# Kernel tuning notes

Hardware: AMD Instinct MI355X
Metric: run time of the kernel (lower is better)

The kernel has to match this reference:

```python
import jax, jax.numpy as jnp
import numpy as np
from jax import lax

IMG_W = 800.0
CONF_THRESHOLD = 0.5
MAX_MATCHES = 8
N_PROPOSALS = 65536
N_TARGETS = 128


def setup_inputs() -> dict:
    key = jax.random.key(0)
    ks = jax.random.split(key, 14)
    N, T = N_PROPOSALS, N_TARGETS
    # raw (pre-normalization) geometric scores: theta in [0, 360) deg,
    # start-point / distance errors in [0, 2*img_w) px (exercises the clamp branch)
    theta = jax.random.uniform(ks[0], (N, T), jnp.float32) * 360.0
    xys = jax.random.uniform(ks[1], (N, T), jnp.float32) * (2.0 * IMG_W)
    dist = jax.random.uniform(ks[2], (N, T), jnp.float32) * (2.0 * IMG_W)
    pos = jax.random.uniform(ks[3], (N, T), jnp.float32)
    neg = jax.random.uniform(ks[4], (N, T), jnp.float32)
    iou = jax.random.uniform(ks[5], (N, T), jnp.float32)
    targets = jax.random.uniform(ks[6], (T, 4), jnp.float32)
    # MatchNet: small MLP 6 -> 64 -> 32 -> 1 with ReLU hidden, sigmoid output
    W1 = jax.random.normal(ks[7], (6, 64), jnp.float32) * 0.3
    b1 = jnp.zeros((64,), jnp.float32)
    W2 = jax.random.normal(ks[8], (64, 32), jnp.float32) * 0.3
    b2 = jnp.zeros((32,), jnp.float32)
    W3 = jax.random.normal(ks[9], (32, 1), jnp.float32) * 0.3
    b3 = jnp.zeros((1,), jnp.float32)
    return {
        "theta_score_deep": theta, "start_xys_score_deep": xys,
        "distances_score_deep": dist, "pos_score_deep": pos,
        "neg_score_deep": neg, "iou_deep": iou, "targets": targets,
        "W1": W1, "b1": b1, "W2": W2, "b2": b2, "W3": W3, "b3": b3,
    }


def _norm(x, cap):
    # torch: x[x > cap] = cap; x = 1 - x / cap
    return 1.0 - jnp.minimum(x, cap) / cap


def _matchnet(feats, W1, b1, W2, b2, W3, b3):
    # feats: [N, T, 6] -> scores [N, T]
    h = jax.nn.relu(feats @ W1 + b1)
    h = jax.nn.relu(h @ W2 + b2)
    return jax.nn.sigmoid(h @ W3 + b3)[..., 0]


def reference(theta_score_deep, start_xys_score_deep, distances_score_deep,
              pos_score_deep, neg_score_deep, iou_deep, targets,
              W1, b1, W2, b2, W3, b3):
    theta = _norm(theta_score_deep, 180.0)
    xys = _norm(start_xys_score_deep, IMG_W)
    dist = _norm(distances_score_deep, IMG_W)
    feats = jnp.stack([theta, xys, dist, pos_score_deep, neg_score_deep, iou_deep],
                      axis=-1)                      # [N, T, 6]
    scores = _matchnet(feats, W1, b1, W2, b2, W3, b3)  # [N, T]
    scores = jnp.where(scores < CONF_THRESHOLD, 0.0, scores)
    # top-k proposals per target, fully batched over the target dim
    vals, idx = lax.top_k(scores.T, MAX_MATCHES)    # [T, K] each
    # the torch loop visits targets in descending order of targets[:, 1]
    order = jnp.argsort(-targets[:, 1], stable=True)  # [T]
    rows = idx[order].reshape(-1).astype(jnp.int32)   # [T*K]
    cols = jnp.repeat(order.astype(jnp.int32), MAX_MATCHES)  # [T*K]
    valid = (vals[order] > 0.0).reshape(-1)           # [T*K] bool
    # fixed-shape padded equivalent of the original's variable-length cat:
    # (rows[valid], cols[valid]) reproduces the torch output exactly
    return rows, cols, valid
```

## Files before the change

kernel.cpp:

```cpp
#include <hip/hip_runtime.h>


typedef unsigned int   u32;
typedef unsigned short u16;
typedef short s8v  __attribute__((ext_vector_type(8)));
typedef float f4v  __attribute__((ext_vector_type(4)));

#define N_PROP   65536
#define N_TGT    128
#define N_PAIR   (N_PROP * N_TGT)
#define CAP      4096
#define MARGIN   0.15f
#define NCHUNK   512

static __device__ __forceinline__ u32 packbf(float a, float b) {
  return __builtin_amdgcn_perm(__float_as_uint(b), __float_as_uint(a), 0x07060302u);
}
static __device__ __forceinline__ float bf16_rne(float x) {
  u32 u = __float_as_uint(x);
  u = u + 0x7fffu + ((u >> 16) & 1u);
  return __uint_as_float(u & 0xffff0000u);
}
static __device__ __forceinline__ float bf2f(u16 u) {
  return __uint_as_float(((u32)u) << 16);
}
static __device__ __forceinline__ s8v mk_frag(u32 a, u32 b, u32 c, u32 d) {
  union { u32 u[4]; s8v v; } x;
  x.u[0] = a; x.u[1] = b; x.u[2] = c; x.u[3] = d;
  return x.v;
}
static __device__ __forceinline__ f4v MF16(s8v a, s8v b, f4v c) {
  return __builtin_amdgcn_mfma_f32_16x16x32_bf16(a, b, c, 0, 0, 0);
}

__global__ __launch_bounds__(256, 4) void k1_mfma(
    const float* __restrict__ p_th, const float* __restrict__ p_xy,
    const float* __restrict__ p_di, const float* __restrict__ p_po,
    const float* __restrict__ p_ne, const float* __restrict__ p_io,
    const float* __restrict__ W1, const float* __restrict__ b1,
    const float* __restrict__ W2, const float* __restrict__ b2,
    const float* __restrict__ W3, const float* __restrict__ b3,
    u16* __restrict__ lgout)
{
  const int tid = threadIdx.x;
  const int l   = tid & 63;
  const int lo4 = l & 15;
  const int q   = (l >> 4) & 3;

  s8v aw1[4];
#pragma unroll
  for (int mt = 0; mt < 4; ++mt) {
    float v[8];
#pragma unroll
    for (int j = 0; j < 8; ++j) {
      const int k = 8 * q + j;
      float x = 0.0f;
      if (k < 6)       x = W1[k * 64 + 16 * mt + lo4];
      else if (k == 6) x = b1[16 * mt + lo4];
      v[j] = bf16_rne(x);
    }
    aw1[mt] = mk_frag(packbf(v[0], v[1]), packbf(v[2], v[3]),
                      packbf(v[4], v[5]), packbf(v[6], v[7]));
  }

  s8v aw2[2][2];
#pragma unroll
  for (int mt = 0; mt < 2; ++mt)
#pragma unroll
    for (int c = 0; c < 2; ++c) {
      float v[8];
#pragma unroll
      for (int j = 0; j < 8; ++j) {
        const int u = 16 * (2 * c + (j >> 2)) + 4 * q + (j & 3);
        v[j] = bf16_rne(W2[u * 32 + 16 * mt + lo4]);
      }
      aw2[mt][c] = mk_frag(packbf(v[0], v[1]), packbf(v[2], v[3]),
                           packbf(v[4], v[5]), packbf(v[6], v[7]));
    }

  float b2l[2][4], w3l[2][4];
#pragma unroll
  for (int mt = 0; mt < 2; ++mt)
#pragma unroll
    for (int r = 0; r < 4; ++r) {
      const int row = 16 * mt + 4 * q + r;
      b2l[mt][r] = b2[row];
      w3l[mt][r] = W3[row];
    }
  const float b3s = b3[0];
  const f4v Z4 = {};

  const bool q0 = (q == 0);

  const int nwaves = (gridDim.x * blockDim.x) >> 6;
  const int w0 = (blockIdx.x * blockDim.x + tid) >> 6;
  const int NGRP = N_PAIR / 16;

#pragma unroll 2
  for (int g = w0; g < NGRP; g += nwaves) {
    const int idx = g * 16 + lo4;
    const float x0 = p_th[idx], x1 = p_xy[idx], x2 = p_di[idx];
    const float x3 = p_po[idx], x4 = p_ne[idx], x5 = p_io[idx];
    const float f0 = fmaf(fminf(x0, 180.0f), -(1.0f / 180.0f), 1.0f);
    const float f1 = fmaf(fminf(x1, 800.0f), -(1.0f / 800.0f), 1.0f);
    const float f2 = fmaf(fminf(x2, 800.0f), -(1.0f / 800.0f), 1.0f);

    const s8v bfeat = mk_frag(q0 ? packbf(f0, f1) : 0u,
                              q0 ? packbf(f2, x3) : 0u,
                              q0 ? packbf(x4, x5) : 0u,
                              q0 ? 0x00003f80u : 0u);

    u32 hl[4], hh[4];
#pragma unroll
    for (int mt = 0; mt < 4; ++mt) {
      const f4v hv = MF16(aw1[mt], bfeat, Z4);
      hl[mt] = packbf(fmaxf(hv[0], 0.0f), fmaxf(hv[1], 0.0f));
      hh[mt] = packbf(fmaxf(hv[2], 0.0f), fmaxf(hv[3], 0.0f));
    }

    const s8v b2f0 = mk_frag(hl[0], hh[0], hl[1], hh[1]);
    const s8v b2f1 = mk_frag(hl[2], hh[2], hl[3], hh[3]);

    f4v acc0 = Z4, acc1 = Z4;
    acc0 = MF16(aw2[0][0], b2f0, acc0);
    acc0 = MF16(aw2[0][1], b2f1, acc0);
    acc1 = MF16(aw2[1][0], b2f0, acc1);
    acc1 = MF16(aw2[1][1], b2f1, acc1);

    float part = 0.0f;
#pragma unroll
    for (int r = 0; r < 4; ++r) {
      part = fmaf(w3l[0][r], fmaxf(acc0[r] + b2l[0][r], 0.0f), part);
      part = fmaf(w3l[1][r], fmaxf(acc1[r] + b2l[1][r], 0.0f), part);
    }
    part += __shfl_xor(part, 16, 64);
    part += __shfl_xor(part, 32, 64);

    if (q0)
      lgout[idx] = (u16)(__float_as_uint(part + b3s) >> 16);
  }
}

__global__ void k2a_part(const u16* __restrict__ lg, float* __restrict__ pval)
{
  const int t = threadIdx.x;
  const int c = blockIdx.x;
  const size_t base = (size_t)c * 128 * 128 + t;
  float v[8];
#pragma unroll
  for (int q = 0; q < 8; ++q) v[q] = -3.4e38f;
#pragma unroll 4
  for (int i = 0; i < 128; ++i) {
    const float x = bf2f(lg[base + (size_t)i * 128]);
    if (x > v[7]) {
      int k = 7;
      while (k > 0 && x > v[k - 1]) { v[k] = v[k - 1]; --k; }
      v[k] = x;
    }
  }
  float* o = pval + ((size_t)c * 128 + t) * 8;
#pragma unroll
  for (int q = 0; q < 8; ++q) o[q] = v[q];
}

__global__ void k2b_merge(const float* __restrict__ pval, float* __restrict__ tau)
{
  __shared__ float sm[64 * 8];
  const int t = blockIdx.x;
  const int i = threadIdx.x;
  float v[8];
#pragma unroll
  for (int q = 0; q < 8; ++q) v[q] = -3.4e38f;
  for (int e = i; e < NCHUNK * 8; e += 64) {
    const float x = pval[(size_t)(e >> 3) * 1024 + (size_t)t * 8 + (e & 7)];
    if (x > v[7]) {
      int k = 7;
      while (k > 0 && x > v[k - 1]) { v[k] = v[k - 1]; --k; }
      v[k] = x;
    }
  }
#pragma unroll
  for (int q = 0; q < 8; ++q) sm[i * 8 + q] = v[q];
  __syncthreads();
  if (i == 0) {
    float w[8];
#pragma unroll
    for (int q = 0; q < 8; ++q) w[q] = -3.4e38f;
    for (int e = 0; e < 512; ++e) {
      const float x = sm[e];
      if (x > w[7]) {
        int k = 7;
        while (k > 0 && x > w[k - 1]) { w[k] = w[k - 1]; --k; }
        w[k] = x;
      }
    }
    tau[t] = w[7] - MARGIN;
  }
}

__global__ void k2c_cand(const u16* __restrict__ lg, const float* __restrict__ tau,
                         int* __restrict__ cnt, int* __restrict__ cand)
{
  const int t = threadIdx.x;
  const int c = blockIdx.x;
  const int n0 = c * 128;
  const float ta = tau[t];
#pragma unroll 4
  for (int i = 0; i < 128; ++i) {
    const int n = n0 + i;
    const float x = bf2f(lg[(size_t)n * 128 + t]);
    if (x >= ta || n < 16) {
      const int p = atomicAdd(&cnt[t], 1);
      if (p < CAP) cand[(size_t)t * CAP + p] = n;
    }
  }
}

__global__ __launch_bounds__(256) void k3_refine(
    const float* __restrict__ p_th, const float* __restrict__ p_xy,
    const float* __restrict__ p_di, const float* __restrict__ p_po,
    const float* __restrict__ p_ne, const float* __restrict__ p_io,
    const float* __restrict__ W1, const float* __restrict__ b1,
    const float* __restrict__ W2, const float* __restrict__ b2,
    const float* __restrict__ W3, const float* __restrict__ b3,
    const int* __restrict__ cnt, const int* __restrict__ cand,
    int* __restrict__ t8i, float* __restrict__ t8k)
{
  __shared__ float wl[2561];
  __shared__ float ck[CAP];
  __shared__ int   cnid[CAP];
  const int t = blockIdx.x;
  const int tid = threadIdx.x;

  for (int i = tid; i < 2561; i += 256) {
    float x;
    if (i < 384)       x = W1[i];
    else if (i < 448)  x = b1[i - 384];
    else if (i < 2496) x = W2[i - 448];
    else if (i < 2528) x = b2[i - 2496];
    else if (i < 2560) x = W3[i - 2528];
    else               x = b3[0];
    wl[i] = x;
  }
  __syncthreads();
  const float* W1L = wl;
  const float* b1L = wl + 384;
  const float* W2L = wl + 448;
  const float* b2L = wl + 2496;
  const float* W3L = wl + 2528;
  const float  b3s = wl[2560];

  int m = cnt[t];
  if (m > CAP) m = CAP;

  for (int i = tid; i < m; i += 256) {
    const int n = cand[(size_t)t * CAP + i];
    const size_t off = (size_t)n * 128 + t;
    float f[6];
    f[0] = 1.0f - fminf(p_th[off], 180.0f) / 180.0f;
    f[1] = 1.0f - fminf(p_xy[off], 800.0f) / 800.0f;
    f[2] = 1.0f - fminf(p_di[off], 800.0f) / 800.0f;
    f[3] = p_po[off]; f[4] = p_ne[off]; f[5] = p_io[off];

    float h1[64];
#pragma unroll
    for (int j = 0; j < 64; ++j) {
      float s = b1L[j];
#pragma unroll
      for (int k = 0; k < 6; ++k) s = fmaf(f[k], W1L[k * 64 + j], s);
      h1[j] = fmaxf(s, 0.0f);
    }
    float h2[32];
#pragma unroll
    for (int j = 0; j < 32; ++j) {
      float s = b2L[j];
#pragma unroll
      for (int k = 0; k < 64; ++k) s = fmaf(h1[k], W2L[k * 32 + j], s);
      h2[j] = fmaxf(s, 0.0f);
    }
    float lo = b3s;
#pragma unroll
    for (int k = 0; k < 32; ++k) lo = fmaf(h2[k], W3L[k], lo);
    const float sg = 1.0f / (1.0f + expf(-lo));
    ck[i]   = (sg < 0.5f) ? 0.0f : sg;
    cnid[i] = n;
  }
  __syncthreads();

  if (tid == 0) {
    float bv[8]; int bi[8];
#pragma unroll
    for (int q = 0; q < 8; ++q) { bv[q] = -1.0f; bi[q] = 0x7fffffff; }
    for (int i = 0; i < m; ++i) {
      const float x = ck[i];
      const int   n = cnid[i];
      if (x > bv[7] || (x == bv[7] && n < bi[7])) {
        int k = 7;
        while (k > 0 && (x > bv[k - 1] || (x == bv[k - 1] && n < bi[k - 1]))) {
          bv[k] = bv[k - 1]; bi[k] = bi[k - 1]; --k;
        }
        bv[k] = x; bi[k] = n;
      }
    }
#pragma unroll
    for (int q = 0; q < 8; ++q) {
      t8i[t * 8 + q] = bi[q];
      t8k[t * 8 + q] = bv[q];
    }
  }
}

__global__ void k4_final(const float* __restrict__ targets,
                         const int* __restrict__ t8i, const float* __restrict__ t8k,
                         int* __restrict__ out)
{
  __shared__ float key[128];
  __shared__ int   ord[128];
  const int i = threadIdx.x;
  key[i] = targets[i * 4 + 1];
  __syncthreads();
  const float ki = key[i];
  int r = 0;
  for (int j = 0; j < 128; ++j) {
    const float kj = key[j];
    r += (kj > ki) || (kj == ki && j < i);
  }
  ord[r] = i;
  __syncthreads();
  const int src = ord[i];
#pragma unroll
  for (int k = 0; k < 8; ++k) {
    out[i * 8 + k]        = t8i[src * 8 + k];
    out[1024 + i * 8 + k] = src;
    out[2048 + i * 8 + k] = (t8k[src * 8 + k] > 0.0f) ? 1 : 0;
  }
}

extern "C" void kernel_launch(void* const* d_in, const int* in_sizes, int n_in,
                              void* d_out, int out_size, void* d_ws, size_t ws_size,
                              hipStream_t stream)
{
  const float* p_th = (const float*)d_in[0];
  const float* p_xy = (const float*)d_in[1];
  const float* p_di = (const float*)d_in[2];
  const float* p_po = (const float*)d_in[3];
  const float* p_ne = (const float*)d_in[4];
  const float* p_io = (const float*)d_in[5];
  const float* tgt  = (const float*)d_in[6];
  const float* W1   = (const float*)d_in[7];
  const float* b1   = (const float*)d_in[8];
  const float* W2   = (const float*)d_in[9];
  const float* b2   = (const float*)d_in[10];
  const float* W3   = (const float*)d_in[11];
  const float* b3   = (const float*)d_in[12];

  char* base = (char*)d_ws;
  u16*   lg   = (u16*)  (base);
  float* pval = (float*)(base + 16777216);
  int*   cand = (int*)  (base + 16777216);
  float* tau  = (float*)(base + 18874368);
  int*   cnt  = (int*)  (base + 18874880);
  int*   t8i  = (int*)  (base + 18875392);
  float* t8k  = (float*)(base + 18879488);

  hipMemsetAsync(cnt, 0, 128 * sizeof(int), stream);

  k1_mfma<<<2048, 256, 0, stream>>>(p_th, p_xy, p_di, p_po, p_ne, p_io,
                                    W1, b1, W2, b2, W3, b3, lg);
  k2a_part<<<NCHUNK, 128, 0, stream>>>(lg, pval);
  k2b_merge<<<128, 64, 0, stream>>>(pval, tau);
  k2c_cand<<<NCHUNK, 128, 0, stream>>>(lg, tau, cnt, cand);
  k3_refine<<<128, 256, 0, stream>>>(p_th, p_xy, p_di, p_po, p_ne, p_io,
                                     W1, b1, W2, b2, W3, b3,
                                     cnt, cand, t8i, t8k);
  k4_final<<<1, 128, 0, stream>>>(tgt, t8i, t8k, (int*)d_out);
}
```

Before: 665.6 us.

## Split refine kernel across blocks per target and coalesce MLP input loads

The refine stage is split into 8 blocks per target. Each block scores a strided slice of the candidates and keeps a partial top-8, and the final kernel merges the 64 partial entries per target. Separately, the MFMA scoring kernel now loads 64 contiguous pairs per wave iteration and redistributes the packed features with shuffles, instead of having each lane group load 16 elements. This is meant to fix the under-occupied 128-block refine kernel, whose single-thread serial top-k scan is long, and to make the global reads fully coalesced. In exchange it adds shuffle overhead and a serial merge step in k4.

```diff
diff --git a/kernel.cpp b/kernel.cpp
--- a/kernel.cpp
+++ b/kernel.cpp
@@ -12,6 +12,8 @@
 #define CAP      4096
 #define MARGIN   0.15f
 #define NCHUNK   512
+#define K3SPLIT  8
+#define SLICE_CAP (CAP / K3SPLIT)
 
 static __device__ __forceinline__ u32 packbf(float a, float b) {
   return __builtin_amdgcn_perm(__float_as_uint(b), __float_as_uint(a), 0x07060302u);
@@ -89,55 +91,61 @@
     }
   const float b3s = b3[0];
   const f4v Z4 = {};
-
   const bool q0 = (q == 0);
 
   const int nwaves = (gridDim.x * blockDim.x) >> 6;
-  const int w0 = (blockIdx.x * blockDim.x + tid) >> 6;
-  const int NGRP = N_PAIR / 16;
-
-#pragma unroll 2
-  for (int g = w0; g < NGRP; g += nwaves) {
-    const int idx = g * 16 + lo4;
-    const float x0 = p_th[idx], x1 = p_xy[idx], x2 = p_di[idx];
-    const float x3 = p_po[idx], x4 = p_ne[idx], x5 = p_io[idx];
+  const int w0i = (blockIdx.x * blockDim.x + tid) >> 6;
+  const int NG64 = N_PAIR / 64;
+
+  for (int g = w0i; g < NG64; g += nwaves) {
+    const int base = g * 64 + l;
+    const float x0 = p_th[base], x1 = p_xy[base], x2 = p_di[base];
+    const float x3 = p_po[base], x4 = p_ne[base], x5 = p_io[base];
     const float f0 = fmaf(fminf(x0, 180.0f), -(1.0f / 180.0f), 1.0f);
     const float f1 = fmaf(fminf(x1, 800.0f), -(1.0f / 800.0f), 1.0f);
     const float f2 = fmaf(fminf(x2, 800.0f), -(1.0f / 800.0f), 1.0f);
-
-    const s8v bfeat = mk_frag(q0 ? packbf(f0, f1) : 0u,
-                              q0 ? packbf(f2, x3) : 0u,
-                              q0 ? packbf(x4, x5) : 0u,
-                              q0 ? 0x00003f80u : 0u);
-
-    u32 hl[4], hh[4];
-#pragma unroll
-    for (int mt = 0; mt < 4; ++mt) {
-      const f4v hv = MF16(aw1[mt], bfeat, Z4);
-      hl[mt] = packbf(fmaxf(hv[0], 0.0f), fmaxf(hv[1], 0.0f));
-      hh[mt] = packbf(fmaxf(hv[2], 0.0f), fmaxf(hv[3], 0.0f));
-    }
-
-    const s8v b2f0 = mk_frag(hl[0], hh[0], hl[1], hh[1]);
-    const s8v b2f1 = mk_frag(hl[2], hh[2], hl[3], hh[3]);
-
-    f4v acc0 = Z4, acc1 = Z4;
-    acc0 = MF16(aw2[0][0], b2f0, acc0);
-    acc0 = MF16(aw2[0][1], b2f1, acc0);
-    acc1 = MF16(aw2[1][0], b2f0, acc1);
-    acc1 = MF16(aw2[1][1], b2f1, acc1);
-
-    float part = 0.0f;
-#pragma unroll
-    for (int r = 0; r < 4; ++r) {
-      part = fmaf(w3l[0][r], fmaxf(acc0[r] + b2l[0][r], 0.0f), part);
-      part = fmaf(w3l[1][r], fmaxf(acc1[r] + b2l[1][r], 0.0f), part);
-    }
-    part += __shfl_xor(part, 16, 64);
-    part += __shfl_xor(part, 32, 64);
-
-    if (q0)
-      lgout[idx] = (u16)(__float_as_uint(part + b3s) >> 16);
+    const u32 pw0 = packbf(f0, f1);
+    const u32 pw1 = packbf(f2, x3);
+    const u32 pw2 = packbf(x4, x5);
+
+#pragma unroll
+    for (int c = 0; c < 4; ++c) {
+      const int s = c * 16 + lo4;
+      const u32 a0 = (u32)__shfl((int)pw0, s, 64);
+      const u32 a1 = (u32)__shfl((int)pw1, s, 64);
+      const u32 a2 = (u32)__shfl((int)pw2, s, 64);
+      const s8v bfeat = mk_frag(q0 ? a0 : 0u, q0 ? a1 : 0u,
+                                q0 ? a2 : 0u, q0 ? 0x00003f80u : 0u);
+
+      u32 hl[4], hh[4];
+#pragma unroll
+      for (int mt = 0; mt < 4; ++mt) {
+        const f4v hv = MF16(aw1[mt], bfeat, Z4);
+        hl[mt] = packbf(fmaxf(hv[0], 0.0f), fmaxf(hv[1], 0.0f));
+        hh[mt] = packbf(fmaxf(hv[2], 0.0f), fmaxf(hv[3], 0.0f));
+      }
+
+      const s8v b2f0 = mk_frag(hl[0], hh[0], hl[1], hh[1]);
+      const s8v b2f1 = mk_frag(hl[2], hh[2], hl[3], hh[3]);
+
+      f4v acc0 = Z4, acc1 = Z4;
+      acc0 = MF16(aw2[0][0], b2f0, acc0);
+      acc0 = MF16(aw2[0][1], b2f1, acc0);
+      acc1 = MF16(aw2[1][0], b2f0, acc1);
+      acc1 = MF16(aw2[1][1], b2f1, acc1);
+
+      float part = 0.0f;
+#pragma unroll
+      for (int r = 0; r < 4; ++r) {
+        part = fmaf(w3l[0][r], fmaxf(acc0[r] + b2l[0][r], 0.0f), part);
+        part = fmaf(w3l[1][r], fmaxf(acc1[r] + b2l[1][r], 0.0f), part);
+      }
+      part += __shfl_xor(part, 16, 64);
+      part += __shfl_xor(part, 32, 64);
+
+      if (q0)
+        lgout[g * 64 + c * 16 + lo4] = (u16)(__float_as_uint(part + b3s) >> 16);
+    }
   }
 }
 
@@ -224,12 +232,13 @@
     const float* __restrict__ W2, const float* __restrict__ b2,
     const float* __restrict__ W3, const float* __restrict__ b3,
     const int* __restrict__ cnt, const int* __restrict__ cand,
-    int* __restrict__ t8i, float* __restrict__ t8k)
+    int* __restrict__ t8i_p, float* __restrict__ t8k_p)
 {
   __shared__ float wl[2561];
-  __shared__ float ck[CAP];
-  __shared__ int   cnid[CAP];
-  const int t = blockIdx.x;
+  __shared__ float ck[SLICE_CAP];
+  __shared__ int   cnid[SLICE_CAP];
+  const int t   = blockIdx.x >> 3;
+  const int b   = blockIdx.x & (K3SPLIT - 1);
   const int tid = threadIdx.x;
 
   for (int i = tid; i < 2561; i += 256) {
@@ -252,8 +261,10 @@
 
   int m = cnt[t];
   if (m > CAP) m = CAP;
-
-  for (int i = tid; i < m; i += 256) {
+  const int mloc = (b < m) ? (m - b + K3SPLIT - 1) / K3SPLIT : 0;
+
+  for (int k = tid; k < mloc; k += 256) {
+    const int i = b + k * K3SPLIT;
     const int n = cand[(size_t)t * CAP + i];
     const size_t off = (size_t)n * 128 + t;
     float f[6];
@@ -267,7 +278,7 @@
     for (int j = 0; j < 64; ++j) {
       float s = b1L[j];
 #pragma unroll
-      for (int k = 0; k < 6; ++k) s = fmaf(f[k], W1L[k * 64 + j], s);
+      for (int k2 = 0; k2 < 6; ++k2) s = fmaf(f[k2], W1L[k2 * 64 + j], s);
       h1[j] = fmaxf(s, 0.0f);
     }
     float h2[32];
@@ -275,15 +286,15 @@
     for (int j = 0; j < 32; ++j) {
       float s = b2L[j];
 #pragma unroll
-      for (int k = 0; k < 64; ++k) s = fmaf(h1[k], W2L[k * 32 + j], s);
+      for (int k2 = 0; k2 < 64; ++k2) s = fmaf(h1[k2], W2L[k2 * 32 + j], s);
       h2[j] = fmaxf(s, 0.0f);
     }
     float lo = b3s;
 #pragma unroll
-    for (int k = 0; k < 32; ++k) lo = fmaf(h2[k], W3L[k], lo);
+    for (int k2 = 0; k2 < 32; ++k2) lo = fmaf(h2[k2], W3L[k2], lo);
     const float sg = 1.0f / (1.0f + expf(-lo));
-    ck[i]   = (sg < 0.5f) ? 0.0f : sg;
-    cnid[i] = n;
+    ck[k]   = (sg < 0.5f) ? 0.0f : sg;
+    cnid[k] = n;
   }
   __syncthreads();
 
@@ -291,7 +302,7 @@
     float bv[8]; int bi[8];
 #pragma unroll
     for (int q = 0; q < 8; ++q) { bv[q] = -1.0f; bi[q] = 0x7fffffff; }
-    for (int i = 0; i < m; ++i) {
+    for (int i = 0; i < mloc; ++i) {
       const float x = ck[i];
       const int   n = cnid[i];
       if (x > bv[7] || (x == bv[7] && n < bi[7])) {
@@ -302,16 +313,18 @@
         bv[k] = x; bi[k] = n;
       }
     }
+    const int o = (t * K3SPLIT + b) * 8;
 #pragma unroll
     for (int q = 0; q < 8; ++q) {
-      t8i[t * 8 + q] = bi[q];
-      t8k[t * 8 + q] = bv[q];
+      t8i_p[o + q] = bi[q];
+      t8k_p[o + q] = bv[q];
     }
   }
 }
 
 __global__ void k4_final(const float* __restrict__ targets,
-                         const int* __restrict__ t8i, const float* __restrict__ t8k,
+                         const int* __restrict__ t8i_p,
+                         const float* __restrict__ t8k_p,
                          int* __restrict__ out)
 {
   __shared__ float key[128];
@@ -328,11 +341,26 @@
   ord[r] = i;
   __syncthreads();
   const int src = ord[i];
+
+  float bv[8]; int bi[8];
+#pragma unroll
+  for (int q = 0; q < 8; ++q) { bv[q] = -1.0f; bi[q] = 0x7fffffff; }
+  for (int e = 0; e < K3SPLIT * 8; ++e) {
+    const float x = t8k_p[src * K3SPLIT * 8 + e];
+    const int   n = t8i_p[src * K3SPLIT * 8 + e];
+    if (x > bv[7] || (x == bv[7] && n < bi[7])) {
+      int k = 7;
+      while (k > 0 && (x > bv[k - 1] || (x == bv[k - 1] && n < bi[k - 1]))) {
+        bv[k] = bv[k - 1]; bi[k] = bi[k - 1]; --k;
+      }
+      bv[k] = x; bi[k] = n;
+    }
+  }
 #pragma unroll
   for (int k = 0; k < 8; ++k) {
-    out[i * 8 + k]        = t8i[src * 8 + k];
+    out[i * 8 + k]        = bi[k];
     out[1024 + i * 8 + k] = src;
-    out[2048 + i * 8 + k] = (t8k[src * 8 + k] > 0.0f) ? 1 : 0;
+    out[2048 + i * 8 + k] = (bv[k] > 0.0f) ? 1 : 0;
   }
 }
 
@@ -355,13 +383,13 @@
   const float* b3   = (const float*)d_in[12];
 
   char* base = (char*)d_ws;
-  u16*   lg   = (u16*)  (base);
-  float* pval = (float*)(base + 16777216);
-  int*   cand = (int*)  (base + 16777216);
-  float* tau  = (float*)(base + 18874368);
-  int*   cnt  = (int*)  (base + 18874880);
-  int*   t8i  = (int*)  (base + 18875392);
-  float* t8k  = (float*)(base + 18879488);
+  u16*   lg    = (u16*)  (base);
+  int*   t8i_p = (int*)  (base);
+  float* t8k_p = (float*)(base + 32768);
+  float* pval  = (float*)(base + 16777216);
+  int*   cand  = (int*)  (base + 16777216);
+  float* tau   = (float*)(base + 18874368);
+  int*   cnt   = (int*)  (base + 18874880);
 
   hipMemsetAsync(cnt, 0, 128 * sizeof(int), stream);
 
@@ -370,8 +398,8 @@
   k2a_part<<<NCHUNK, 128, 0, stream>>>(lg, pval);
   k2b_merge<<<128, 64, 0, stream>>>(pval, tau);
   k2c_cand<<<NCHUNK, 128, 0, stream>>>(lg, tau, cnt, cand);
-  k3_refine<<<128, 256, 0, stream>>>(p_th, p_xy, p_di, p_po, p_ne, p_io,
-                                     W1, b1, W2, b2, W3, b3,
-                                     cnt, cand, t8i, t8k);
-  k4_final<<<1, 128, 0, stream>>>(tgt, t8i, t8k, (int*)d_out);
-}
+  k3_refine<<<N_TGT * K3SPLIT, 256, 0, stream>>>(p_th, p_xy, p_di, p_po, p_ne,
+                                                 p_io, W1, b1, W2, b2, W3, b3,
+                                                 cnt, cand, t8i_p, t8k_p);
+  k4_final<<<1, 128, 0, stream>>>(tgt, t8i_p, t8k_p, (int*)d_out);
+}
```

After: 706.9 us. 6.2% more time.
